# Optimization experiments

Measured on AMD Instinct MI355X. Metric: run time of the kernel, lower is better.

Reference implementation:

```python
import jax, jax.numpy as jnp
import numpy as np

N_NODES = 50000
N_EDGES = 800000
DIMS = [128, 128, 128, 64]  # in, hid1, hid2, out
EPS = 1e-12


def setup_inputs() -> dict:
    key = jax.random.key(0)
    ks = jax.random.split(key, 32)
    inp = {
        "x": jax.random.normal(ks[0], (N_NODES, DIMS[0]), dtype=jnp.float32),
        "edge_src": jax.random.randint(ks[1], (N_EDGES,), 0, N_NODES),
        "edge_dst": jax.random.randint(ks[2], (N_EDGES,), 0, N_NODES),
    }
    k = 3
    for l in range(3):
        din, dout = DIMS[l], DIMS[l + 1]
        s_in = 1.0 / np.sqrt(din)
        inp[f"Wp{l+1}"] = jax.random.uniform(ks[k], (din, din), jnp.float32, -s_in, s_in); k += 1
        inp[f"bp{l+1}"] = jax.random.uniform(ks[k], (din,), jnp.float32, -s_in, s_in); k += 1
        inp[f"Ws{l+1}"] = jax.random.uniform(ks[k], (din, dout), jnp.float32, -s_in, s_in); k += 1
        inp[f"Wn{l+1}"] = jax.random.uniform(ks[k], (din, dout), jnp.float32, -s_in, s_in); k += 1
        inp[f"b{l+1}"] = jnp.zeros((dout,), jnp.float32); k += 1
    return inp


def _sage_pool_layer(x, src, dst, Wp, bp, Ws, Wn, b):
    # per-edge: relu(fc_pool(x_src)); [E, din]
    m = jax.nn.relu(x[src] @ Wp + bp)
    # max-pool over in-neighbors of each dst node; [N, din]
    pooled = jax.ops.segment_max(m, dst, num_segments=x.shape[0])
    deg = jax.ops.segment_sum(jnp.ones((dst.shape[0],), x.dtype), dst,
                              num_segments=x.shape[0])
    pooled = jnp.where(deg[:, None] > 0, pooled, 0.0)  # zero-degree -> 0 (DGL)
    return x @ Ws + pooled @ Wn + b


def _l2norm_relu(h):
    n = jnp.sqrt(jnp.sum(h * h, axis=1, keepdims=True))
    return jax.nn.relu(h / jnp.maximum(n, EPS))


def reference(x, edge_src, edge_dst,
              Wp1, bp1, Ws1, Wn1, b1,
              Wp2, bp2, Ws2, Wn2, b2,
              Wp3, bp3, Ws3, Wn3, b3):
    h = _l2norm_relu(_sage_pool_layer(x, edge_src, edge_dst, Wp1, bp1, Ws1, Wn1, b1))
    h = _l2norm_relu(_sage_pool_layer(h, edge_src, edge_dst, Wp2, bp2, Ws2, Wn2, b2))
    h = _l2norm_relu(_sage_pool_layer(h, edge_src, edge_dst, Wp3, bp3, Ws3, Wn3, b3))
    return h
```

## Files before the change

kernel.cpp:

```cpp
#include <hip/hip_runtime.h>
#include <math.h>

#define N_NODES 50000
#define N_EDGES 800000
#define CAP 64
#define RANGES 8
#define NODES_PER_RANGE 6250
#define GEMMB 782
#define CSRB (N_EDGES / 256 * RANGES)
#define LROW 136

typedef __attribute__((ext_vector_type(8))) short short8;
typedef __attribute__((ext_vector_type(4))) short short4v;
typedef __attribute__((ext_vector_type(4))) float f32x4;

__device__ __forceinline__ unsigned short f2bf(float f) {
    unsigned int u = __float_as_uint(f);
    return (unsigned short)((u + 0x7FFFu + ((u >> 16) & 1u)) >> 16);
}

template <bool F32>
__device__ __forceinline__ short8 loadA(const void* A, int off) {
    short8 r;
    if (F32) {
        const float* p = (const float*)A + off;
        float4 f0 = *(const float4*)p;
        float4 f1 = *(const float4*)(p + 4);
        r[0] = (short)f2bf(f0.x); r[1] = (short)f2bf(f0.y);
        r[2] = (short)f2bf(f0.z); r[3] = (short)f2bf(f0.w);
        r[4] = (short)f2bf(f1.x); r[5] = (short)f2bf(f1.y);
        r[6] = (short)f2bf(f1.z); r[7] = (short)f2bf(f1.w);
    } else {
        r = *(const short8*)((const unsigned short*)A + off);
    }
    return r;
}

struct WDescs { const float* W[9]; int N[9]; };

__global__ __launch_bounds__(256) void prep_kernel(
    WDescs wd, unsigned short* __restrict__ Wpk, int* __restrict__ deg)
{
    const int nthr = gridDim.x * 256;
    const int tid = blockIdx.x * 256 + threadIdx.x;
    for (int id = tid; id < 9 * 16384; id += nthr) {
        int mi = id >> 14;
        int loc = id & 16383;
        int N = wd.N[mi];
        if (loc < 128 * N) {
            int c = loc / (N * 32);
            int n = (loc - c * N * 32) >> 5;
            int k = c * 32 + (loc & 31);
            Wpk[mi * 16384 + loc] = f2bf(wd.W[mi][k * N + n]);
        }
    }
    for (int i = tid; i < N_NODES; i += nthr) deg[i] = 0;
}

__global__ __launch_bounds__(256) void mix_kernel(
    const int* __restrict__ esrc, const int* __restrict__ edst,
    int* __restrict__ deg, unsigned short* __restrict__ csr16,
    const float* __restrict__ x, const unsigned short* __restrict__ Wp1,
    const float* __restrict__ bp1, unsigned short* __restrict__ Y)
{
    if (blockIdx.x >= GEMMB) {
        int b = blockIdx.x - GEMMB;
        int range = b & (RANGES - 1);
        int e = (b >> 3) * 256 + threadIdx.x;
        int d = edst[e];
        if ((unsigned)(d - range * NODES_PER_RANGE) < (unsigned)NODES_PER_RANGE) {
            int r = atomicAdd(&deg[d], 1);
            if (r < CAP) csr16[(d << 6) + r] = (unsigned short)esrc[e];
        }
        return;
    }
    const int tile = blockIdx.x;
    const int lane = threadIdx.x & 63;
    const int wv = threadIdx.x >> 6;
    const int cl = lane & 15;
    const int quad = lane >> 4;
    const int rowBase = tile * 64 + wv * 16;
    const int ar = min(rowBase + cl, N_NODES - 1);
    const int bLane = cl * 32 + quad * 8;

    f32x4 acc[8];
    #pragma unroll
    for (int t = 0; t < 8; ++t) acc[t] = (f32x4){0.f, 0.f, 0.f, 0.f};

    #pragma unroll
    for (int c = 0; c < 4; ++c) {
        short8 af = loadA<true>(x, ar * 128 + c * 32 + quad * 8);
        const unsigned short* Bc = Wp1 + c * 4096 + bLane;
        #pragma unroll
        for (int t = 0; t < 8; ++t) {
            short8 bf = *(const short8*)(Bc + t * 512);
            acc[t] = __builtin_amdgcn_mfma_f32_16x16x32_bf16(af, bf, acc[t], 0, 0, 0);
        }
    }
    const int row0 = rowBase + quad * 4;
    #pragma unroll
    for (int t = 0; t < 8; ++t) {
        float bc = bp1[t * 16 + cl];
        #pragma unroll
        for (int g = 0; g < 4; ++g) {
            int r = row0 + g;
            if (r < N_NODES)
                Y[r * 128 + t * 16 + cl] = f2bf(fmaxf(acc[t][g] + bc, 0.0f));
        }
    }
}

__global__ __launch_bounds__(256) void pool_max4(
    const unsigned short* __restrict__ y, const int* __restrict__ deg,
    const unsigned short* __restrict__ csr16, unsigned short* __restrict__ pool)
{
    const int wv = threadIdx.x >> 6;
    const int lane = threadIdx.x & 63;
    const int half = lane >> 5;
    const int q = lane & 31;
    const int n = blockIdx.x * 4 + wv;
    const int e0 = n << 6;
    const int e1 = e0 + min(deg[n], CAP);
    const unsigned short* yb = y + 4 * q;

    short4v acc = (short4v){0, 0, 0, 0};
    int e = e0;
    for (; e + 8 <= e1; e += 8) {
        uint2 I = *(const uint2*)(csr16 + e + (half << 2));
        int sa = (int)(I.x & 0xFFFF), sb = (int)(I.x >> 16);
        int sc = (int)(I.y & 0xFFFF), sd = (int)(I.y >> 16);
        short4v va = *(const short4v*)(yb + (sa << 7));
        short4v vb = *(const short4v*)(yb + (sb << 7));
        short4v vc = *(const short4v*)(yb + (sc << 7));
        short4v vd = *(const short4v*)(yb + (sd << 7));
        acc = __builtin_elementwise_max(acc, va);
        acc = __builtin_elementwise_max(acc, vb);
        acc = __builtin_elementwise_max(acc, vc);
        acc = __builtin_elementwise_max(acc, vd);
    }
    for (; e < e1; ++e) {
        int s = csr16[e];
        short4v v = *(const short4v*)(yb + (s << 7));
        acc = __builtin_elementwise_max(acc, v);
    }
    int2 ai = *(int2*)&acc;
    int2 bi;
    bi.x = __shfl_xor(ai.x, 32, 64);
    bi.y = __shfl_xor(ai.y, 32, 64);
    short4v other = *(short4v*)&bi;
    acc = __builtin_elementwise_max(acc, other);
    if (half == 0)
        *(short4v*)(pool + n * 128 + 4 * q) = acc;
}

template <bool A0F32, bool LAST>
__global__ __launch_bounds__(256) void dualy_kernel(
    const void* __restrict__ A0,
    const unsigned short* __restrict__ B0, const unsigned short* __restrict__ B1,
    const float* __restrict__ bias,
    const unsigned short* __restrict__ PL,
    unsigned short* __restrict__ outH, float* __restrict__ outF,
    const unsigned short* __restrict__ Bnext, const float* __restrict__ bnext,
    unsigned short* __restrict__ Yout)
{
    constexpr int NT = LAST ? 4 : 8;
    constexpr int N = NT * 16;
    __shared__ unsigned short lds[4][16 * LROW];

    const int lane = threadIdx.x & 63;
    const int wv = threadIdx.x >> 6;
    const int cl = lane & 15;
    const int quad = lane >> 4;
    const int nodeBase = blockIdx.x * 64 + wv * 16;
    unsigned short* plw = &lds[wv][0];

    const int ar = min(nodeBase + cl, N_NODES - 1);
    const int aBase = ar * 128 + quad * 8;
    const int bLane = cl * 32 + quad * 8;

    f32x4 acc[NT];
    #pragma unroll
    for (int t = 0; t < NT; ++t) acc[t] = (f32x4){0.f, 0.f, 0.f, 0.f};

    #pragma unroll
    for (int c = 0; c < 4; ++c) {
        short8 a0 = loadA<A0F32>(A0, aBase + c * 32);
        short8 a1 = *(const short8*)(PL + aBase + c * 32);
        const unsigned short* B0c = B0 + c * (N * 32) + bLane;
        const unsigned short* B1c = B1 + c * (N * 32) + bLane;
        #pragma unroll
        for (int t = 0; t < NT; ++t) {
            short8 bf = *(const short8*)(B0c + t * 512);
            acc[t] = __builtin_amdgcn_mfma_f32_16x16x32_bf16(a0, bf, acc[t], 0, 0, 0);
        }
        #pragma unroll
        for (int t = 0; t < NT; ++t) {
            short8 bf = *(const short8*)(B1c + t * 512);
            acc[t] = __builtin_amdgcn_mfma_f32_16x16x32_bf16(a1, bf, acc[t], 0, 0, 0);
        }
    }

    #pragma unroll
    for (int t = 0; t < NT; ++t) {
        float bc = bias[t * 16 + cl];
        #pragma unroll
        for (int g = 0; g < 4; ++g) acc[t][g] += bc;
    }

    float inv[4];
    #pragma unroll
    for (int g = 0; g < 4; ++g) {
        float s = 0.f;
        #pragma unroll
        for (int t = 0; t < NT; ++t) s += acc[t][g] * acc[t][g];
        s += __shfl_xor(s, 1, 64);
        s += __shfl_xor(s, 2, 64);
        s += __shfl_xor(s, 4, 64);
        s += __shfl_xor(s, 8, 64);
        inv[g] = 1.0f / fmaxf(sqrtf(s), 1e-12f);
    }

    const int row0 = nodeBase + quad * 4;

    if (LAST) {
        #pragma unroll
        for (int t = 0; t < NT; ++t)
            #pragma unroll
            for (int g = 0; g < 4; ++g) {
                int r = row0 + g;
                if (r < N_NODES)
                    outF[r * N + t * 16 + cl] = fmaxf(acc[t][g] * inv[g], 0.0f);
            }
        return;
    }

    #pragma unroll
    for (int t = 0; t < NT; ++t)
        #pragma unroll
        for (int g = 0; g < 4; ++g) {
            int r = row0 + g;
            unsigned short h = f2bf(fmaxf(acc[t][g] * inv[g], 0.0f));
            if (r < N_NODES) outH[r * 128 + t * 16 + cl] = h;
            plw[(quad * 4 + g) * LROW + t * 16 + cl] = h;
        }

    f32x4 ya[8];
    #pragma unroll
    for (int t = 0; t < 8; ++t) ya[t] = (f32x4){0.f, 0.f, 0.f, 0.f};
    #pragma unroll
    for (int c = 0; c < 4; ++c) {
        short8 af = *(const short8*)(plw + cl * LROW + c * 32 + quad * 8);
        const unsigned short* Bc = Bnext + c * 4096 + bLane;
        #pragma unroll
        for (int t = 0; t < 8; ++t) {
            short8 bf = *(const short8*)(Bc + t * 512);
            ya[t] = __builtin_amdgcn_mfma_f32_16x16x32_bf16(af, bf, ya[t], 0, 0, 0);
        }
    }
    #pragma unroll
    for (int t = 0; t < 8; ++t) {
        float bc = bnext[t * 16 + cl];
        #pragma unroll
        for (int g = 0; g < 4; ++g) {
            int r = row0 + g;
            if (r < N_NODES)
                Yout[r * 128 + t * 16 + cl] = f2bf(fmaxf(ya[t][g] + bc, 0.0f));
        }
    }
}

extern "C" void kernel_launch(void* const* d_in, const int* in_sizes, int n_in,
                              void* d_out, int out_size, void* d_ws, size_t ws_size,
                              hipStream_t stream) {
    const float* x    = (const float*)d_in[0];
    const int*   esrc = (const int*)d_in[1];
    const int*   edst = (const int*)d_in[2];
    const float* Wp[3], *bp[3], *Ws[3], *Wn[3], *bb[3];
    for (int l = 0; l < 3; ++l) {
        Wp[l] = (const float*)d_in[3 + 5 * l];
        bp[l] = (const float*)d_in[4 + 5 * l];
        Ws[l] = (const float*)d_in[5 + 5 * l];
        Wn[l] = (const float*)d_in[6 + 5 * l];
        bb[l] = (const float*)d_in[7 + 5 * l];
    }

    const int NF = N_NODES * 128;
    unsigned short* YA  = (unsigned short*)d_ws;
    unsigned short* YB  = YA + NF;
    unsigned short* PL  = YB + NF;
    unsigned short* H1  = PL + NF;
    unsigned short* H2  = H1 + NF;
    unsigned short* Wpk = H2 + NF;
    int* deg = (int*)(Wpk + 9 * 16384);
    unsigned short* csr16 = (unsigned short*)(deg + N_NODES);

    auto WH = [&](int i) { return Wpk + i * 16384; };

    WDescs wd;
    wd.W[0] = Wp[0]; wd.N[0] = 128;
    wd.W[1] = Ws[0]; wd.N[1] = 128;
    wd.W[2] = Wn[0]; wd.N[2] = 128;
    wd.W[3] = Wp[1]; wd.N[3] = 128;
    wd.W[4] = Ws[1]; wd.N[4] = 128;
    wd.W[5] = Wn[1]; wd.N[5] = 128;
    wd.W[6] = Wp[2]; wd.N[6] = 128;
    wd.W[7] = Ws[2]; wd.N[7] = 64;
    wd.W[8] = Wn[2]; wd.N[8] = 64;

    const int poolBlocks = N_NODES / 4;

    prep_kernel<<<576, 256, 0, stream>>>(wd, Wpk, deg);
    mix_kernel<<<GEMMB + CSRB, 256, 0, stream>>>(esrc, edst, deg, csr16,
                                                 x, WH(0), bp[0], YA);
    pool_max4<<<poolBlocks, 256, 0, stream>>>(YA, deg, csr16, PL);
    dualy_kernel<true, false><<<GEMMB, 256, 0, stream>>>(
        x, WH(1), WH(2), bb[0], PL, H1, nullptr, WH(3), bp[1], YB);
    pool_max4<<<poolBlocks, 256, 0, stream>>>(YB, deg, csr16, PL);
    dualy_kernel<false, false><<<GEMMB, 256, 0, stream>>>(
        H1, WH(4), WH(5), bb[1], PL, H2, nullptr, WH(6), bp[2], YA);
    pool_max4<<<poolBlocks, 256, 0, stream>>>(YA, deg, csr16, PL);
    dualy_kernel<false, true><<<GEMMB, 256, 0, stream>>>(
        H2, WH(7), WH(8), bb[2], PL, nullptr, (float*)d_out,
        nullptr, nullptr, nullptr);
}
```

Before: 348.9 us.

## Split GEMM output columns across wave pairs and double block count

The GEMM blocks in mix_kernel and dualy_kernel now cover 32 rows instead of 64, with two waves sharing each 16-row group and each computing half the output columns. The launch uses twice as many blocks, aiming for more parallelism and fewer accumulator registers per wave on the 256-CU device. The row L2 norm now needs a cross-wave partial-sum exchange through shared memory, and the fused next-layer GEMM needs a __syncthreads barrier. Each wave also reloads the same A rows, which duplicates A traffic.

```diff
diff --git a/kernel.cpp b/kernel.cpp
--- a/kernel.cpp
+++ b/kernel.cpp
@@ -6,7 +6,7 @@
 #define CAP 64
 #define RANGES 8
 #define NODES_PER_RANGE 6250
-#define GEMMB 782
+#define GEMMB2 1563
 #define CSRB (N_EDGES / 256 * RANGES)
 #define LROW 136
 
@@ -63,8 +63,8 @@
     const float* __restrict__ x, const unsigned short* __restrict__ Wp1,
     const float* __restrict__ bp1, unsigned short* __restrict__ Y)
 {
-    if (blockIdx.x >= GEMMB) {
-        int b = blockIdx.x - GEMMB;
+    if (blockIdx.x >= GEMMB2) {
+        int b = blockIdx.x - GEMMB2;
         int range = b & (RANGES - 1);
         int e = (b >> 3) * 256 + threadIdx.x;
         int d = edst[e];
@@ -74,38 +74,39 @@
         }
         return;
     }
-    const int tile = blockIdx.x;
     const int lane = threadIdx.x & 63;
     const int wv = threadIdx.x >> 6;
+    const int rg = wv >> 1;
+    const int ch = wv & 1;
     const int cl = lane & 15;
     const int quad = lane >> 4;
-    const int rowBase = tile * 64 + wv * 16;
+    const int rowBase = blockIdx.x * 32 + rg * 16;
     const int ar = min(rowBase + cl, N_NODES - 1);
     const int bLane = cl * 32 + quad * 8;
 
-    f32x4 acc[8];
-    #pragma unroll
-    for (int t = 0; t < 8; ++t) acc[t] = (f32x4){0.f, 0.f, 0.f, 0.f};
+    f32x4 acc[4];
+    #pragma unroll
+    for (int t = 0; t < 4; ++t) acc[t] = (f32x4){0.f, 0.f, 0.f, 0.f};
 
     #pragma unroll
     for (int c = 0; c < 4; ++c) {
         short8 af = loadA<true>(x, ar * 128 + c * 32 + quad * 8);
         const unsigned short* Bc = Wp1 + c * 4096 + bLane;
         #pragma unroll
-        for (int t = 0; t < 8; ++t) {
-            short8 bf = *(const short8*)(Bc + t * 512);
+        for (int t = 0; t < 4; ++t) {
+            short8 bf = *(const short8*)(Bc + (ch * 4 + t) * 512);
             acc[t] = __builtin_amdgcn_mfma_f32_16x16x32_bf16(af, bf, acc[t], 0, 0, 0);
         }
     }
     const int row0 = rowBase + quad * 4;
     #pragma unroll
-    for (int t = 0; t < 8; ++t) {
-        float bc = bp1[t * 16 + cl];
+    for (int t = 0; t < 4; ++t) {
+        float bc = bp1[(ch * 4 + t) * 16 + cl];
         #pragma unroll
         for (int g = 0; g < 4; ++g) {
             int r = row0 + g;
             if (r < N_NODES)
-                Y[r * 128 + t * 16 + cl] = f2bf(fmaxf(acc[t][g] + bc, 0.0f));
+                Y[r * 128 + (ch * 4 + t) * 16 + cl] = f2bf(fmaxf(acc[t][g] + bc, 0.0f));
         }
     }
 }
@@ -163,108 +164,120 @@
     const unsigned short* __restrict__ Bnext, const float* __restrict__ bnext,
     unsigned short* __restrict__ Yout)
 {
-    constexpr int NT = LAST ? 4 : 8;
-    constexpr int N = NT * 16;
-    __shared__ unsigned short lds[4][16 * LROW];
+    constexpr int NTD = LAST ? 2 : 4;
+    constexpr int NOUT = LAST ? 64 : 128;
+    __shared__ unsigned short hT[2][16 * LROW];
+    __shared__ float ps[2][16][2];
 
     const int lane = threadIdx.x & 63;
     const int wv = threadIdx.x >> 6;
+    const int rg = wv >> 1;
+    const int ch = wv & 1;
     const int cl = lane & 15;
     const int quad = lane >> 4;
-    const int nodeBase = blockIdx.x * 64 + wv * 16;
-    unsigned short* plw = &lds[wv][0];
-
-    const int ar = min(nodeBase + cl, N_NODES - 1);
+    const int rowBase = blockIdx.x * 32 + rg * 16;
+
+    const int ar = min(rowBase + cl, N_NODES - 1);
     const int aBase = ar * 128 + quad * 8;
     const int bLane = cl * 32 + quad * 8;
 
-    f32x4 acc[NT];
-    #pragma unroll
-    for (int t = 0; t < NT; ++t) acc[t] = (f32x4){0.f, 0.f, 0.f, 0.f};
+    f32x4 acc[NTD];
+    #pragma unroll
+    for (int t = 0; t < NTD; ++t) acc[t] = (f32x4){0.f, 0.f, 0.f, 0.f};
 
     #pragma unroll
     for (int c = 0; c < 4; ++c) {
         short8 a0 = loadA<A0F32>(A0, aBase + c * 32);
         short8 a1 = *(const short8*)(PL + aBase + c * 32);
-        const unsigned short* B0c = B0 + c * (N * 32) + bLane;
-        const unsigned short* B1c = B1 + c * (N * 32) + bLane;
-        #pragma unroll
-        for (int t = 0; t < NT; ++t) {
-            short8 bf = *(const short8*)(B0c + t * 512);
+        const unsigned short* B0c = B0 + c * (NOUT * 32) + bLane;
+        const unsigned short* B1c = B1 + c * (NOUT * 32) + bLane;
+        #pragma unroll
+        for (int t = 0; t < NTD; ++t) {
+            short8 bf = *(const short8*)(B0c + (ch * NTD + t) * 512);
             acc[t] = __builtin_amdgcn_mfma_f32_16x16x32_bf16(a0, bf, acc[t], 0, 0, 0);
         }
         #pragma unroll
-        for (int t = 0; t < NT; ++t) {
-            short8 bf = *(const short8*)(B1c + t * 512);
+        for (int t = 0; t < NTD; ++t) {
+            short8 bf = *(const short8*)(B1c + (ch * NTD + t) * 512);
             acc[t] = __builtin_amdgcn_mfma_f32_16x16x32_bf16(a1, bf, acc[t], 0, 0, 0);
         }
     }
 
     #pragma unroll
-    for (int t = 0; t < NT; ++t) {
-        float bc = bias[t * 16 + cl];
+    for (int t = 0; t < NTD; ++t) {
+        float bc = bias[(ch * NTD + t) * 16 + cl];
         #pragma unroll
         for (int g = 0; g < 4; ++g) acc[t][g] += bc;
     }
 
-    float inv[4];
     #pragma unroll
     for (int g = 0; g < 4; ++g) {
         float s = 0.f;
         #pragma unroll
-        for (int t = 0; t < NT; ++t) s += acc[t][g] * acc[t][g];
+        for (int t = 0; t < NTD; ++t) s += acc[t][g] * acc[t][g];
         s += __shfl_xor(s, 1, 64);
         s += __shfl_xor(s, 2, 64);
         s += __shfl_xor(s, 4, 64);
         s += __shfl_xor(s, 8, 64);
-        inv[g] = 1.0f / fmaxf(sqrtf(s), 1e-12f);
-    }
-
-    const int row0 = nodeBase + quad * 4;
+        if (cl == 0) ps[rg][quad * 4 + g][ch] = s;
+    }
+    __syncthreads();
+
+    float inv[4];
+    #pragma unroll
+    for (int g = 0; g < 4; ++g) {
+        float tot = ps[rg][quad * 4 + g][0] + ps[rg][quad * 4 + g][1];
+        inv[g] = 1.0f / fmaxf(sqrtf(tot), 1e-12f);
+    }
+
+    const int row0 = rowBase + quad * 4;
 
     if (LAST) {
         #pragma unroll
-        for (int t = 0; t < NT; ++t)
+        for (int t = 0; t < NTD; ++t)
             #pragma unroll
             for (int g = 0; g < 4; ++g) {
                 int r = row0 + g;
                 if (r < N_NODES)
-                    outF[r * N + t * 16 + cl] = fmaxf(acc[t][g] * inv[g], 0.0f);
+                    outF[r * NOUT + (ch * NTD + t) * 16 + cl] =
+                        fmaxf(acc[t][g] * inv[g], 0.0f);
             }
         return;
     }
 
     #pragma unroll
-    for (int t = 0; t < NT; ++t)
+    for (int t = 0; t < NTD; ++t)
         #pragma unroll
         for (int g = 0; g < 4; ++g) {
             int r = row0 + g;
             unsigned short h = f2bf(fmaxf(acc[t][g] * inv[g], 0.0f));
-            if (r < N_NODES) outH[r * 128 + t * 16 + cl] = h;
-            plw[(quad * 4 + g) * LROW + t * 16 + cl] = h;
-        }
-
-    f32x4 ya[8];
-    #pragma unroll
-    for (int t = 0; t < 8; ++t) ya[t] = (f32x4){0.f, 0.f, 0.f, 0.f};
+            if (r < N_NODES) outH[r * 128 + (ch * NTD + t) * 16 + cl] = h;
+            hT[rg][(quad * 4 + g) * LROW + (ch * NTD + t) * 16 + cl] = h;
+        }
+    __syncthreads();
+
+    f32x4 ya[4];
+    #pragma unroll
+    for (int t = 0; t < 4; ++t) ya[t] = (f32x4){0.f, 0.f, 0.f, 0.f};
     #pragma unroll
     for (int c = 0; c < 4; ++c) {
-        short8 af = *(const short8*)(plw + cl * LROW + c * 32 + quad * 8);
+        short8 af = *(const short8*)(&hT[rg][cl * LROW + c * 32 + quad * 8]);
         const unsigned short* Bc = Bnext + c * 4096 + bLane;
         #pragma unroll
-        for (int t = 0; t < 8; ++t) {
-            short8 bf = *(const short8*)(Bc + t * 512);
+        for (int t = 0; t < 4; ++t) {
+            short8 bf = *(const short8*)(Bc + (ch * 4 + t) * 512);
             ya[t] = __builtin_amdgcn_mfma_f32_16x16x32_bf16(af, bf, ya[t], 0, 0, 0);
         }
     }
     #pragma unroll
-    for (int t = 0; t < 8; ++t) {
-        float bc = bnext[t * 16 + cl];
+    for (int t = 0; t < 4; ++t) {
+        float bc = bnext[(ch * 4 + t) * 16 + cl];
         #pragma unroll
         for (int g = 0; g < 4; ++g) {
             int r = row0 + g;
             if (r < N_NODES)
-                Yout[r * 128 + t * 16 + cl] = f2bf(fmaxf(ya[t][g] + bc, 0.0f));
+                Yout[r * 128 + (ch * 4 + t) * 16 + cl] =
+                    f2bf(fmaxf(ya[t][g] + bc, 0.0f));
         }
     }
 }
@@ -310,16 +323,16 @@
     const int poolBlocks = N_NODES / 4;
 
     prep_kernel<<<576, 256, 0, stream>>>(wd, Wpk, deg);
-    mix_kernel<<<GEMMB + CSRB, 256, 0, stream>>>(esrc, edst, deg, csr16,
-                                                 x, WH(0), bp[0], YA);
+    mix_kernel<<<GEMMB2 + CSRB, 256, 0, stream>>>(esrc, edst, deg, csr16,
+                                                  x, WH(0), bp[0], YA);
     pool_max4<<<poolBlocks, 256, 0, stream>>>(YA, deg, csr16, PL);
-    dualy_kernel<true, false><<<GEMMB, 256, 0, stream>>>(
+    dualy_kernel<true, false><<<GEMMB2, 256, 0, stream>>>(
         x, WH(1), WH(2), bb[0], PL, H1, nullptr, WH(3), bp[1], YB);
     pool_max4<<<poolBlocks, 256, 0, stream>>>(YB, deg, csr16, PL);
-    dualy_kernel<false, false><<<GEMMB, 256, 0, stream>>>(
+    dualy_kernel<false, false><<<GEMMB2, 256, 0, stream>>>(
         H1, WH(4), WH(5), bb[1], PL, H2, nullptr, WH(6), bp[2], YA);
     pool_max4<<<poolBlocks, 256, 0, stream>>>(YA, deg, csr16, PL);
-    dualy_kernel<false, true><<<GEMMB, 256, 0, stream>>>(
+    dualy_kernel<false, true><<<GEMMB2, 256, 0, stream>>>(
         H2, WH(7), WH(8), bb[2], PL, nullptr, (float*)d_out,
         nullptr, nullptr, nullptr);
 }
```

Measured after the change: 350.3 us. About the same (+0.4%).
